# Kernel optimization log

Hardware: AMD Instinct MI355X
Metric: run time of the kernel (lower is better)

## Reference

```python
import jax, jax.numpy as jnp
import numpy as np
import math

R, C, B, E, H, F = 64, 256, 1, 768, 12, 3072
D = E // H  # head dim = 64
EPS = 1e-6  # flax LayerNorm default


def _ln(x, s, b):
    mu = jnp.mean(x, axis=-1, keepdims=True)
    var = jnp.mean((x - mu) ** 2, axis=-1, keepdims=True)
    return (x - mu) * jax.lax.rsqrt(var + EPS) * s + b


def setup_inputs() -> dict:
    key = jax.random.key(0)
    ks = jax.random.split(key, 16)
    w = lambda k, sh: jax.random.normal(k, sh, jnp.float32) * 0.02
    z = lambda sh: jnp.zeros(sh, jnp.float32)
    return {
        "x": jax.random.normal(ks[0], (R, C, B, E), jnp.float32),
        "ln1_s": jnp.ones((E,), jnp.float32), "ln1_b": z((E,)),
        "r_wq": w(ks[1], (E, E)), "r_bq": z((E,)),
        "r_wk": w(ks[2], (E, E)), "r_bk": z((E,)),
        "r_wv": w(ks[3], (E, E)), "r_bv": z((E,)),
        "r_wo": w(ks[4], (E, E)), "r_bo": z((E,)),
        "ln2_s": jnp.ones((E,), jnp.float32), "ln2_b": z((E,)),
        "c_wq": w(ks[5], (E, E)), "c_bq": z((E,)),
        "c_wk": w(ks[6], (E, E)), "c_bk": z((E,)),
        "c_wv": w(ks[7], (E, E)), "c_bv": z((E,)),
        "c_wo": w(ks[8], (E, E)), "c_bo": z((E,)),
        "ln3_s": jnp.ones((E,), jnp.float32), "ln3_b": z((E,)),
        "f_w1": w(ks[9], (E, F)), "f_b1": z((F,)),
        "f_w2": w(ks[10], (F, E)), "f_b2": z((E,)),
    }


def reference(x, ln1_s, ln1_b, r_wq, r_bq, r_wk, r_bk, r_wv, r_bv, r_wo, r_bo,
              ln2_s, ln2_b, c_wq, c_bq, c_wk, c_bk, c_wv, c_bv, c_wo, c_bo,
              ln3_s, ln3_b, f_w1, f_b1, f_w2, f_b2):
    qkv = (R, C, B, H, D)
    # --- tied row self-attention (NOTE: original code has no residual adds) ---
    h = _ln(x, ln1_s, ln1_b)
    q = (h @ r_wq + r_bq).reshape(qkv) * (D ** -0.5 / math.sqrt(R))  # tied-row scaling
    k = (h @ r_wk + r_bk).reshape(qkv)
    v = (h @ r_wv + r_bv).reshape(qkv)
    aw = jnp.einsum('rinhd,rjnhd->hnij', q, k)  # single softmax tied across rows
    ap = jax.nn.softmax(aw, axis=-1)
    ctx = jnp.einsum('hnij,rjnhd->rinhd', ap, v).reshape(R, C, B, E)
    x = ctx @ r_wo + r_bo
    # --- column self-attention (per-column attention over rows) ---
    h = _ln(x, ln2_s, ln2_b)
    q = (h @ c_wq + c_bq).reshape(qkv) * (D ** -0.5)
    k = (h @ c_wk + c_bk).reshape(qkv)
    v = (h @ c_wv + c_bv).reshape(qkv)
    aw = jnp.einsum('icnhd,jcnhd->hcnij', q, k)
    ap = jax.nn.softmax(aw, axis=-1)
    ctx = jnp.einsum('hcnij,jcnhd->icnhd', ap, v).reshape(R, C, B, E)
    x = ctx @ c_wo + c_bo
    # --- FFN (gelu approximate=True matches flax default) ---
    h = _ln(x, ln3_s, ln3_b)
    return jax.nn.gelu(h @ f_w1 + f_b1) @ f_w2 + f_b2
```

## Files before the change

kernel.cpp:

```cpp
#include <hip/hip_runtime.h>
#include <hip/hip_bf16.h>
#include <stdint.h>
#include <stddef.h>

#define R_ 64
#define C_ 256
#define E_ 768
#define H_ 12
#define F_ 3072
#define D_ 64
#define NT_ (R_*C_)
#define HCRD_ ((size_t)H_*C_*R_*D_)

typedef float f32x4 __attribute__((ext_vector_type(4)));
typedef __bf16 bf16x8 __attribute__((ext_vector_type(8)));
typedef unsigned short us4 __attribute__((ext_vector_type(4)));
typedef unsigned short us8 __attribute__((ext_vector_type(8)));

typedef __attribute__((address_space(3))) uint32_t lds_u32;
typedef __attribute__((address_space(1))) uint32_t glb_u32;

__device__ __forceinline__ void gld16(const uint16_t* g, uint16_t* l) {
  __builtin_amdgcn_global_load_lds((const glb_u32*)g, (lds_u32*)l, 16, 0, 0);
}

__device__ __forceinline__ uint16_t f2b(float f) {
  __bf16 h = (__bf16)f;
  return *(uint16_t*)&h;
}

#define VM_WAIT4 { asm volatile("s_waitcnt vmcnt(4)" ::: "memory"); __builtin_amdgcn_sched_barrier(0); }
#define VM_WAIT0 { asm volatile("s_waitcnt vmcnt(0)" ::: "memory"); __builtin_amdgcn_sched_barrier(0); }
#define BARRIER  { __builtin_amdgcn_s_barrier(); __builtin_amdgcn_sched_barrier(0); }

enum { EP_F32B = 0, EP_GELU = 1, EP_AW = 2, EP_CTX = 3, EP_QKVROW = 4, EP_QKVCOL = 5 };

template<int EP, bool SWZ, bool PERM>
__global__ __launch_bounds__(256)
void gemm_bt(const uint16_t* __restrict__ A, const uint16_t* __restrict__ B,
             const float* __restrict__ bias, const float* __restrict__ biasK,
             const float* __restrict__ biasV, void* __restrict__ out,
             int M, int N, int K, int lda, int ldb, long sAz, long sBz, float scale)
{
  __shared__ uint16_t As[3][4096];
  __shared__ uint16_t Bs[3][4096];
  const int tid  = threadIdx.x;
  const int wave = tid >> 6, lane = tid & 63;
  const int z = blockIdx.z;

  int bx = blockIdx.x, by = blockIdx.y;
  if constexpr (SWZ) {
    int lin = blockIdx.x + gridDim.x * blockIdx.y;
    const int q = (gridDim.x * gridDim.y) >> 3;
    const int wid = (lin & 7) * q + (lin >> 3);
    bx = wid % gridDim.x; by = wid / gridDim.x;
  }

  const long bm = (long)by * 128;
  int kc = 0; long bnb = bx;
  if constexpr (EP == EP_AW) { kc = bx & 3; bnb = bx >> 2; }
  const long bn = bnb * 128;
  const uint16_t* Bb = B + (long)z * sBz + bn * (long)ldb + (long)kc * 1024;
  const int wr = (wave >> 1) * 64;
  const int wc = (wave & 1) * 64;
  const int lr = lane & 15;
  const int lq = lane >> 4;

  const int t0 = tid, t1 = tid + 256;
  const int ar0 = t0 >> 2, ar1 = t1 >> 2;
  const int ac0 = (((t0 & 3) ^ ((ar0 >> 1) & 3)) * 8);
  const int ac1 = (((t1 & 3) ^ ((ar1 >> 1) & 3)) * 8);

  long am0 = bm + ar0, am1 = bm + ar1;
  if constexpr (PERM) {
    am0 = ((am0 & 63) << 8) | (am0 >> 6);
    am1 = ((am1 & 63) << 8) | (am1 >> 6);
  }
  const uint16_t* a0p = A + (long)z * sAz + am0 * (long)lda + (long)kc * 1024;
  const uint16_t* a1p = A + (long)z * sAz + am1 * (long)lda + (long)kc * 1024;
  const uint16_t* b0p = Bb + (long)ar0 * ldb;
  const uint16_t* b1p = Bb + (long)ar1 * ldb;

  auto STAGE = [&](int bi, int kt) {
    gld16(a0p + kt + ac0, &As[bi][t0 * 8]);
    gld16(a1p + kt + ac1, &As[bi][t1 * 8]);
    gld16(b0p + kt + ac0, &Bs[bi][t0 * 8]);
    gld16(b1p + kt + ac1, &Bs[bi][t1 * 8]);
  };

  int apos[4], bpos[4];
#pragma unroll
  for (int i = 0; i < 4; ++i) {
    const int ra = wr + i * 16 + lr;
    const int rb = wc + i * 16 + lr;
    apos[i] = ra * 32 + (lq ^ ((ra >> 1) & 3)) * 8;
    bpos[i] = rb * 32 + (lq ^ ((rb >> 1) & 3)) * 8;
  }

  f32x4 acc[4][4];
#pragma unroll
  for (int i = 0; i < 4; ++i)
#pragma unroll
    for (int j = 0; j < 4; ++j) acc[i][j] = (f32x4){0.f, 0.f, 0.f, 0.f};

  const int nt = K >> 5;
  STAGE(0, 0);
  if (nt > 1) { STAGE(1, 32); VM_WAIT4; } else { VM_WAIT0; }
  BARRIER;

  int cur = 0;
  for (int t = 0; t < nt; ++t) {
    if (t + 2 < nt) {
      int sl = cur + 2; if (sl >= 3) sl -= 3;
      STAGE(sl, (t + 2) << 5);
    }

    bf16x8 af[4], bfm[4];
#pragma unroll
    for (int i = 0; i < 4; ++i) {
      af[i]  = *(const bf16x8*)&As[cur][apos[i]];
      bfm[i] = *(const bf16x8*)&Bs[cur][bpos[i]];
    }
    __builtin_amdgcn_s_setprio(1);
#pragma unroll
    for (int mi = 0; mi < 4; ++mi)
#pragma unroll
      for (int ni = 0; ni < 4; ++ni)
        acc[mi][ni] = __builtin_amdgcn_mfma_f32_16x16x32_bf16(af[mi], bfm[ni], acc[mi][ni], 0, 0, 0);
    __builtin_amdgcn_s_setprio(0);

    if (t + 2 < nt)      { VM_WAIT4; BARRIER; }
    else if (t + 1 < nt) { VM_WAIT0; BARRIER; }
    cur = (cur == 2) ? 0 : cur + 1;
  }
  __syncthreads();

  if constexpr (EP == EP_F32B) {
#pragma unroll
    for (int mi = 0; mi < 4; ++mi)
#pragma unroll
      for (int ni = 0; ni < 4; ++ni)
#pragma unroll
        for (int r = 0; r < 4; ++r) {
          const long row = bm + wr + mi * 16 + lq * 4 + r;
          const long col = bn + wc + ni * 16 + lr;
          ((float*)out)[row * N + col] = acc[mi][ni][r] + bias[col];
        }
  } else if constexpr (EP == EP_AW) {
#pragma unroll
    for (int mi = 0; mi < 4; ++mi)
#pragma unroll
      for (int ni = 0; ni < 4; ++ni)
#pragma unroll
        for (int r = 0; r < 4; ++r) {
          const long row = bm + wr + mi * 16 + lq * 4 + r;
          const long col = bn + wc + ni * 16 + lr;
          ((float*)out)[((long)(z * 4 + kc) * M + row) * N + col] = acc[mi][ni][r];
        }
  } else if constexpr (EP == EP_CTX) {
#pragma unroll
    for (int mi = 0; mi < 4; ++mi)
#pragma unroll
      for (int ni = 0; ni < 4; ++ni)
#pragma unroll
        for (int r = 0; r < 4; ++r) {
          const long row = bm + wr + mi * 16 + lq * 4 + r;
          const long col = bn + wc + ni * 16 + lr;
          ((uint16_t*)out)[((col >> 6) * C_ + row) * E_ + (long)z * 64 + (col & 63)] =
              f2b(acc[mi][ni][r]);
        }
  } else {
    uint16_t* slab = (wave < 3) ? &As[wave][0] : &Bs[0][0];
    const long colb = bn + wc;
    int grp = 0; long cc0 = colb;
    const float* bb = bias;
    if constexpr (EP != EP_GELU) {
      grp = colb >= 1536 ? 2 : (colb >= 768 ? 1 : 0);
      cc0 = colb - (long)grp * 768;
      bb = grp == 0 ? bias : (grp == 1 ? biasK : biasV);
    }
    const bool tr = (EP != EP_GELU) && (grp == 2);

#pragma unroll
    for (int mi = 0; mi < 4; ++mi)
#pragma unroll
      for (int ni = 0; ni < 4; ++ni)
#pragma unroll
        for (int r = 0; r < 4; ++r) {
          const int lrow = mi * 16 + lq * 4 + r;
          const int lcol = ni * 16 + lr;
          float val;
          if constexpr (EP == EP_GELU) {
            const float t = acc[mi][ni][r] + bias[colb + lcol];
            const float u = 0.7978845608028654f * (t + 0.044715f * t * t * t);
            const float e = __expf(2.f * u);
            val = 0.5f * t * (2.f - 2.f / (e + 1.f));
          } else {
            val = acc[mi][ni][r] + bb[cc0 + lcol];
            if (grp == 0) val *= scale;
          }
          const int sr = tr ? lcol : lrow;
          const int sc = tr ? lrow : lcol;
          const int psc = (sc & 7) | ((((sc >> 3) ^ (sr & 7))) << 3);
          slab[sr * 64 + psc] = f2b(val);
        }

    uint16_t* o16 = (uint16_t*)out;
    long obase, rstride;
    if constexpr (EP == EP_GELU) {
      obase = (bm + wr) * (long)N + colb; rstride = N;
    } else {
      const long h = cc0 >> 6;
      const long m0 = bm + wr;
      if constexpr (EP == EP_QKVROW) {
        const long rr = m0 >> 8, c0 = m0 & 255;
        if (grp < 2) { obase = (size_t)grp * HCRD_ + ((h * C_ + c0) * R_ + rr) * D_; rstride = R_ * D_; }
        else         { obase = 2 * HCRD_ + ((h * R_ + rr) * D_) * C_ + c0;           rstride = C_; }
      } else {
        const long cq = m0 >> 6;
        if (grp < 2) { obase = (size_t)grp * HCRD_ + ((h * C_ + cq) * R_) * D_; rstride = D_; }
        else         { obase = 2 * HCRD_ + ((h * C_ + cq) * D_) * R_;           rstride = R_; }
      }
    }

    const int rl = lane >> 3, chn = lane & 7;
#pragma unroll
    for (int pp = 0; pp < 8; ++pp) {
      const int srow = pp * 8 + rl;
      const int pch = chn ^ (srow & 7);
      us8 wv = *(const us8*)&slab[srow * 64 + pch * 8];
      *(us8*)(o16 + obase + (long)srow * rstride + chn * 8) = wv;
    }
  }
}

__global__ __launch_bounds__(256)
void ln_k(const float* __restrict__ x, const float* __restrict__ s, const float* __restrict__ b,
          uint16_t* __restrict__ out)
{
  const int wave = threadIdx.x >> 6, lane = threadIdx.x & 63;
  const long row = (long)blockIdx.x * 4 + wave;
  const float* xr = x + row * E_;
  f32x4 v[3];
  float sum = 0.f, sq = 0.f;
#pragma unroll
  for (int i = 0; i < 3; ++i) {
    v[i] = *(const f32x4*)(xr + (i * 64 + lane) * 4);
#pragma unroll
    for (int j = 0; j < 4; ++j) { sum += v[i][j]; sq += v[i][j] * v[i][j]; }
  }
#pragma unroll
  for (int m = 1; m < 64; m <<= 1) { sum += __shfl_xor(sum, m); sq += __shfl_xor(sq, m); }
  const float mu = sum * (1.f / E_);
  const float var = sq * (1.f / E_) - mu * mu;
  const float rs = rsqrtf(var + 1e-6f);
  uint16_t* orow = out + row * E_;
#pragma unroll
  for (int i = 0; i < 3; ++i) {
    const int e0 = (i * 64 + lane) * 4;
    us4 o;
#pragma unroll
    for (int j = 0; j < 4; ++j) o[j] = f2b((v[i][j] - mu) * rs * s[e0 + j] + b[e0 + j]);
    *(us4*)(orow + e0) = o;
  }
}

__global__ __launch_bounds__(256)
void softmax_k4(const float* __restrict__ aw4, uint16_t* __restrict__ ap)
{
  const int wave = threadIdx.x >> 6, lane = threadIdx.x & 63;
  const long row = (long)blockIdx.x * 4 + wave;
  const long h = row >> 8, i = row & 255;
  f32x4 v = (f32x4){0.f, 0.f, 0.f, 0.f};
#pragma unroll
  for (int kc = 0; kc < 4; ++kc) {
    f32x4 t = *(const f32x4*)(aw4 + (((h * 4 + kc) * C_ + i) * C_) + lane * 4);
#pragma unroll
    for (int j = 0; j < 4; ++j) v[j] += t[j];
  }
  float m = fmaxf(fmaxf(v[0], v[1]), fmaxf(v[2], v[3]));
#pragma unroll
  for (int k = 1; k < 64; k <<= 1) m = fmaxf(m, __shfl_xor(m, k));
  f32x4 e; float s = 0.f;
#pragma unroll
  for (int j = 0; j < 4; ++j) { e[j] = __expf(v[j] - m); s += e[j]; }
#pragma unroll
  for (int k = 1; k < 64; k <<= 1) s += __shfl_xor(s, k);
  const float inv = 1.f / s;
  us4 o;
#pragma unroll
  for (int j = 0; j < 4; ++j) o[j] = f2b(e[j] * inv);
  *(us4*)(ap + row * C_ + lane * 4) = o;
}

__global__ __launch_bounds__(256)
void tcvt(const float* __restrict__ in, uint16_t* __restrict__ out, int K, int N)
{
  __shared__ float t[32][33];
  const int tx = threadIdx.x, ty = threadIdx.y;
  const long k0 = (long)blockIdx.y * 32, n0 = (long)blockIdx.x * 32;
  for (int i = ty; i < 32; i += 8) t[i][tx] = in[(k0 + i) * N + n0 + tx];
  __syncthreads();
  for (int i = ty; i < 32; i += 8) out[(n0 + i) * K + k0 + tx] = f2b(t[tx][i]);
}

__global__ __launch_bounds__(64)
void colattn(const uint16_t* __restrict__ q, const uint16_t* __restrict__ k,
             const uint16_t* __restrict__ v, uint16_t* __restrict__ ctx)
{
  __shared__ uint16_t Qs[64 * 64];
  __shared__ uint16_t Ks[64 * 64];
  __shared__ uint16_t Vs[64 * 64];
  const int hc = blockIdx.x;
  const int h = hc >> 8, c = hc & 255;
  const int lane = threadIdx.x;
  const uint16_t* qb = q + (long)hc * (R_ * D_);
  const uint16_t* kb = k + (long)hc * (R_ * D_);
  const uint16_t* vb = v + (long)hc * (D_ * R_);
#pragma unroll
  for (int it = 0; it < 8; ++it) {
    const int o = (it * 64 + lane) * 8;
    gld16(qb + o, &Qs[o]);
    gld16(kb + o, &Ks[o]);
    gld16(vb + o, &Vs[o]);
  }
  asm volatile("s_waitcnt vmcnt(0)" ::: "memory");
  __builtin_amdgcn_sched_barrier(0);

  const int lr = lane & 15, lq = lane >> 4;
  f32x4 acc[4][4];
#pragma unroll
  for (int i = 0; i < 4; ++i)
#pragma unroll
    for (int j = 0; j < 4; ++j) acc[i][j] = (f32x4){0.f, 0.f, 0.f, 0.f};

#pragma unroll
  for (int kt = 0; kt < 2; ++kt) {
    bf16x8 af[4], bfm[4];
#pragma unroll
    for (int i = 0; i < 4; ++i) {
      af[i]  = *(const bf16x8*)&Qs[(i * 16 + lr) * 64 + kt * 32 + lq * 8];
      bfm[i] = *(const bf16x8*)&Ks[(i * 16 + lr) * 64 + kt * 32 + lq * 8];
    }
#pragma unroll
    for (int mi = 0; mi < 4; ++mi)
#pragma unroll
      for (int ni = 0; ni < 4; ++ni)
        acc[mi][ni] = __builtin_amdgcn_mfma_f32_16x16x32_bf16(af[mi], bfm[ni], acc[mi][ni], 0, 0, 0);
  }

#pragma unroll
  for (int mi = 0; mi < 4; ++mi) {
#pragma unroll
    for (int r = 0; r < 4; ++r) {
      float mx = fmaxf(fmaxf(acc[mi][0][r], acc[mi][1][r]), fmaxf(acc[mi][2][r], acc[mi][3][r]));
#pragma unroll
      for (int s = 1; s < 16; s <<= 1) mx = fmaxf(mx, __shfl_xor(mx, s));
      float e0 = __expf(acc[mi][0][r] - mx), e1 = __expf(acc[mi][1][r] - mx);
      float e2 = __expf(acc[mi][2][r] - mx), e3 = __expf(acc[mi][3][r] - mx);
      float sum = e0 + e1 + e2 + e3;
#pragma unroll
      for (int s = 1; s < 16; s <<= 1) sum += __shfl_xor(sum, s);
      const float inv = 1.f / sum;
      const int i = mi * 16 + lq * 4 + r;
      Qs[i * 64 +  0 + lr] = f2b(e0 * inv);
      Qs[i * 64 + 16 + lr] = f2b(e1 * inv);
      Qs[i * 64 + 32 + lr] = f2b(e2 * inv);
      Qs[i * 64 + 48 + lr] = f2b(e3 * inv);
    }
  }
  __syncthreads();

  f32x4 o_[4][4];
#pragma unroll
  for (int i = 0; i < 4; ++i)
#pragma unroll
    for (int j = 0; j < 4; ++j) o_[i][j] = (f32x4){0.f, 0.f, 0.f, 0.f};

#pragma unroll
  for (int kt = 0; kt < 2; ++kt) {
    bf16x8 pa[4], vv[4];
#pragma unroll
    for (int i = 0; i < 4; ++i) {
      pa[i] = *(const bf16x8*)&Qs[(i * 16 + lr) * 64 + kt * 32 + lq * 8];
      vv[i] = *(const bf16x8*)&Vs[(i * 16 + lr) * 64 + kt * 32 + lq * 8];
    }
#pragma unroll
    for (int mi = 0; mi < 4; ++mi)
#pragma unroll
      for (int ni = 0; ni < 4; ++ni)
        o_[mi][ni] = __builtin_amdgcn_mfma_f32_16x16x32_bf16(pa[mi], vv[ni], o_[mi][ni], 0, 0, 0);
  }

#pragma unroll
  for (int mi = 0; mi < 4; ++mi)
#pragma unroll
    for (int ni = 0; ni < 4; ++ni)
#pragma unroll
      for (int r = 0; r < 4; ++r) {
        const int i = mi * 16 + lq * 4 + r;
        const int d = ni * 16 + lr;
        ctx[((long)i * C_ + c) * E_ + h * 64 + d] = f2b(o_[mi][ni][r]);
      }
}

extern "C" void kernel_launch(void* const* d_in, const int* in_sizes, int n_in,
                              void* d_out, int out_size, void* d_ws, size_t ws_size,
                              hipStream_t stream)
{
  (void)in_sizes; (void)n_in; (void)out_size; (void)ws_size;
  const float* x     = (const float*)d_in[0];
  const float* ln1_s = (const float*)d_in[1];
  const float* ln1_b = (const float*)d_in[2];
  const float* r_wq  = (const float*)d_in[3];
  const float* r_bq  = (const float*)d_in[4];
  const float* r_wk  = (const float*)d_in[5];
  const float* r_bk  = (const float*)d_in[6];
  const float* r_wv  = (const float*)d_in[7];
  const float* r_bv  = (const float*)d_in[8];
  const float* r_wo  = (const float*)d_in[9];
  const float* r_bo  = (const float*)d_in[10];
  const float* ln2_s = (const float*)d_in[11];
  const float* ln2_b = (const float*)d_in[12];
  const float* c_wq  = (const float*)d_in[13];
  const float* c_bq  = (const float*)d_in[14];
  const float* c_wk  = (const float*)d_in[15];
  const float* c_bk  = (const float*)d_in[16];
  const float* c_wv  = (const float*)d_in[17];
  const float* c_bv  = (const float*)d_in[18];
  const float* c_wo  = (const float*)d_in[19];
  const float* c_bo  = (const float*)d_in[20];
  const float* ln3_s = (const float*)d_in[21];
  const float* ln3_b = (const float*)d_in[22];
  const float* f_w1  = (const float*)d_in[23];
  const float* f_b1  = (const float*)d_in[24];
  const float* f_w2  = (const float*)d_in[25];
  const float* f_b2  = (const float*)d_in[26];

  uint8_t* p = (uint8_t*)d_ws;
  auto take = [&p](size_t n) { uint8_t* r = p; p += (n + 255) & ~(size_t)255; return r; };

  uint16_t* wqkv1 = (uint16_t*)take((size_t)3 * E_ * E_ * 2);
  uint16_t* wqkv2 = (uint16_t*)take((size_t)3 * E_ * E_ * 2);
  uint16_t* rwoT  = (uint16_t*)take((size_t)E_ * E_ * 2);
  uint16_t* cwoT  = (uint16_t*)take((size_t)E_ * E_ * 2);
  uint16_t* w1T   = (uint16_t*)take((size_t)E_ * F_ * 2);
  uint16_t* w2T   = (uint16_t*)take((size_t)F_ * E_ * 2);
  uint16_t* hb    = (uint16_t*)take((size_t)NT_ * E_ * 2);
  uint16_t* qkvT  = (uint16_t*)take(3 * HCRD_ * 2);
  uint16_t* qT = qkvT, *kT = qkvT + HCRD_, *vT = qkvT + 2 * HCRD_;
  uint16_t* ctxb  = (uint16_t*)take((size_t)NT_ * E_ * 2);
  uint16_t* apb   = (uint16_t*)take((size_t)H_ * C_ * C_ * 2);
  uint16_t* g     = qkvT;
  float*    awb4  = (float*)ctxb;
  float*    x1    = (float*)d_out;

  const dim3 tb32(32, 8);
  const dim3 gEE(E_ / 32, E_ / 32);
  tcvt<<<gEE, tb32, 0, stream>>>(r_wq, wqkv1 + 0 * E_ * E_, E_, E_);
  tcvt<<<gEE, tb32, 0, stream>>>(r_wk, wqkv1 + 1 * E_ * E_, E_, E_);
  tcvt<<<gEE, tb32, 0, stream>>>(r_wv, wqkv1 + 2 * E_ * E_, E_, E_);
  tcvt<<<gEE, tb32, 0, stream>>>(c_wq, wqkv2 + 0 * E_ * E_, E_, E_);
  tcvt<<<gEE, tb32, 0, stream>>>(c_wk, wqkv2 + 1 * E_ * E_, E_, E_);
  tcvt<<<gEE, tb32, 0, stream>>>(c_wv, wqkv2 + 2 * E_ * E_, E_, E_);
  tcvt<<<gEE, tb32, 0, stream>>>(r_wo, rwoT, E_, E_);
  tcvt<<<gEE, tb32, 0, stream>>>(c_wo, cwoT, E_, E_);
  tcvt<<<dim3(F_ / 32, E_ / 32), tb32, 0, stream>>>(f_w1, w1T, E_, F_);
  tcvt<<<dim3(E_ / 32, F_ / 32), tb32, 0, stream>>>(f_w2, w2T, F_, E_);

  const dim3 gProj(E_ / 128, NT_ / 128, 1);
  const dim3 gQKV((3 * E_) / 128, NT_ / 128, 1);

  ln_k<<<NT_ / 4, 256, 0, stream>>>(x, ln1_s, ln1_b, hb);
  gemm_bt<EP_QKVROW, true, false><<<gQKV, 256, 0, stream>>>(hb, wqkv1, r_bq, r_bk, r_bv, qkvT,
      NT_, 3 * E_, E_, E_, E_, 0, 0, 0.015625f);
  gemm_bt<EP_AW, false, false><<<dim3(8, C_ / 128, H_), 256, 0, stream>>>(
      qT, kT, nullptr, nullptr, nullptr, awb4,
      C_, C_, 1024, R_ * D_, R_ * D_, (long)C_ * R_ * D_, (long)C_ * R_ * D_, 1.f);
  softmax_k4<<<(H_ * C_) / 4, 256, 0, stream>>>(awb4, apb);
  gemm_bt<EP_CTX, false, false><<<dim3((R_ * D_) / 128, C_ / 128, H_), 256, 0, stream>>>(
      apb, vT, nullptr, nullptr, nullptr,
      ctxb, C_, R_ * D_, C_, C_, C_, (long)C_ * C_, (long)R_ * D_ * C_, 1.f);
  gemm_bt<EP_F32B, true, false><<<gProj, 256, 0, stream>>>(ctxb, rwoT, r_bo, nullptr, nullptr, x1,
      NT_, E_, E_, E_, E_, 0, 0, 1.f);

  ln_k<<<NT_ / 4, 256, 0, stream>>>(x1, ln2_s, ln2_b, hb);
  gemm_bt<EP_QKVCOL, true, true><<<gQKV, 256, 0, stream>>>(hb, wqkv2, c_bq, c_bk, c_bv, qkvT,
      NT_, 3 * E_, E_, E_, E_, 0, 0, 0.125f);
  colattn<<<H_ * C_, 64, 0, stream>>>(qT, kT, vT, ctxb);
  gemm_bt<EP_F32B, true, false><<<gProj, 256, 0, stream>>>(ctxb, cwoT, c_bo, nullptr, nullptr, x1,
      NT_, E_, E_, E_, E_, 0, 0, 1.f);

  ln_k<<<NT_ / 4, 256, 0, stream>>>(x1, ln3_s, ln3_b, hb);
  gemm_bt<EP_GELU, true, false><<<dim3(F_ / 128, NT_ / 128, 1), 256, 0, stream>>>(
      hb, w1T, f_b1, nullptr, nullptr, g,
      NT_, F_, E_, E_, E_, 0, 0, 1.f);
  gemm_bt<EP_F32B, true, false><<<gProj, 256, 0, stream>>>(g, w2T, f_b2, nullptr, nullptr, d_out,
      NT_, E_, F_, F_, F_, 0, 0, 1.f);
}
```

Measured before the change: 596.6 us.

## Add 256x256-tile 8-wave GEMM kernel for projection, QKV and FFN GEMMs

Adds a gemm256 kernel using 512 threads, 256x256 output tiles and a K=64 double-buffered LDS pipeline. Each K step is split into four half-stages, with loads interleaved between MFMA groups. All large token-dimension GEMMs (QKV, output projections, FFN) now use it, which raises arithmetic intensity per block and cuts global traffic. The old 128-tile kernel is trimmed to only the batched attention GEMMs. The large tiles produce few blocks for the N=768 GEMMs (192 blocks), which may underfill the GPU, and they increase register pressure.

```diff
diff --git a/kernel.cpp b/kernel.cpp
--- a/kernel.cpp
+++ b/kernel.cpp
@@ -29,18 +29,221 @@
   return *(uint16_t*)&h;
 }
 
+#define VM_WAIT6 { asm volatile("s_waitcnt vmcnt(6)" ::: "memory"); __builtin_amdgcn_sched_barrier(0); }
 #define VM_WAIT4 { asm volatile("s_waitcnt vmcnt(4)" ::: "memory"); __builtin_amdgcn_sched_barrier(0); }
 #define VM_WAIT0 { asm volatile("s_waitcnt vmcnt(0)" ::: "memory"); __builtin_amdgcn_sched_barrier(0); }
 #define BARRIER  { __builtin_amdgcn_s_barrier(); __builtin_amdgcn_sched_barrier(0); }
 
 enum { EP_F32B = 0, EP_GELU = 1, EP_AW = 2, EP_CTX = 3, EP_QKVROW = 4, EP_QKVCOL = 5 };
 
-template<int EP, bool SWZ, bool PERM>
+template<int EP, bool PERM>
+__global__ __launch_bounds__(512, 2)
+void gemm256(const uint16_t* __restrict__ A, const uint16_t* __restrict__ B,
+             const float* __restrict__ bias, const float* __restrict__ biasK,
+             const float* __restrict__ biasV, void* __restrict__ out,
+             int N, int K, int lda, int ldb, float scale)
+{
+  __shared__ uint16_t lds[2][4][8192];
+  const int tid  = threadIdx.x;
+  const int wave = tid >> 6, lane = tid & 63;
+  const int wm = wave >> 2, wn = wave & 3;
+  const int lr = lane & 15, lq = lane >> 4;
+
+  int lin = blockIdx.x + gridDim.x * blockIdx.y;
+  const int q8 = (gridDim.x * gridDim.y) >> 3;
+  const int wid = (lin & 7) * q8 + (lin >> 3);
+  const int bx = wid % gridDim.x, by = wid / gridDim.x;
+  const long bm = (long)by * 256, bn = (long)bx * 256;
+
+  const int r0 = tid >> 2;
+  const int csw = (((tid & 3) ^ ((r0 >> 1) & 3)) * 8);
+  long am0 = bm + r0, am1 = bm + r0 + 128;
+  if constexpr (PERM) {
+    am0 = ((am0 & 63) << 8) | (am0 >> 6);
+    am1 = ((am1 & 63) << 8) | (am1 >> 6);
+  }
+  const uint16_t* aR0 = A + am0 * (long)lda + csw;
+  const uint16_t* aR1 = A + am1 * (long)lda + csw;
+  const uint16_t* bR0 = B + (bn + r0) * (long)ldb + csw;
+  const uint16_t* bR1 = B + (bn + r0 + 128) * (long)ldb + csw;
+
+  auto stageH = [&](int s) {
+    const int u = s >> 2, j = s & 3;
+    const int kb = u * 64 + (j >> 1) * 32;
+    uint16_t* d = &lds[u & 1][j][0];
+    if (j & 1) { gld16(aR0 + kb, d + tid * 8); gld16(aR1 + kb, d + (tid + 512) * 8); }
+    else       { gld16(bR0 + kb, d + tid * 8); gld16(bR1 + kb, d + (tid + 512) * 8); }
+  };
+  auto aoff = [&](int row) { return row * 32 + ((lq ^ ((row >> 1) & 3)) * 8); };
+
+  f32x4 acc[8][4];
+#pragma unroll
+  for (int i = 0; i < 8; ++i)
+#pragma unroll
+    for (int j = 0; j < 4; ++j) acc[i][j] = (f32x4){0.f, 0.f, 0.f, 0.f};
+
+  const int nt = K >> 6;
+  stageH(0); stageH(1); stageH(2); stageH(3);
+  VM_WAIT4;
+  stageH(4); stageH(5); stageH(6);
+  VM_WAIT6;
+  BARRIER;
+
+  for (int t = 0; t < nt; ++t) {
+    const int buf = t & 1;
+    const uint16_t* B0h = &lds[buf][0][0];
+    const uint16_t* A0h = &lds[buf][1][0];
+    const uint16_t* B1h = &lds[buf][2][0];
+    const uint16_t* A1h = &lds[buf][3][0];
+    const int s0 = 4 * t + 7;
+    bf16x8 af[4], bf[4];
+
+#pragma unroll
+    for (int i = 0; i < 4; ++i) {
+      bf[i] = *(const bf16x8*)&B0h[aoff(wn * 64 + i * 16 + lr)];
+      af[i] = *(const bf16x8*)&A0h[aoff(wm * 128 + i * 16 + lr)];
+    }
+    if (s0 < 4 * nt) stageH(s0);
+    BARRIER;
+    __builtin_amdgcn_s_setprio(1);
+#pragma unroll
+    for (int mi = 0; mi < 4; ++mi)
+#pragma unroll
+      for (int ni = 0; ni < 4; ++ni)
+        acc[mi][ni] = __builtin_amdgcn_mfma_f32_16x16x32_bf16(af[mi], bf[ni], acc[mi][ni], 0, 0, 0);
+    __builtin_amdgcn_s_setprio(0);
+    BARRIER;
+
+#pragma unroll
+    for (int i = 0; i < 4; ++i)
+      af[i] = *(const bf16x8*)&A0h[aoff(wm * 128 + 64 + i * 16 + lr)];
+    if (s0 + 1 < 4 * nt) stageH(s0 + 1);
+    BARRIER;
+    __builtin_amdgcn_s_setprio(1);
+#pragma unroll
+    for (int mi = 0; mi < 4; ++mi)
+#pragma unroll
+      for (int ni = 0; ni < 4; ++ni)
+        acc[4 + mi][ni] = __builtin_amdgcn_mfma_f32_16x16x32_bf16(af[mi], bf[ni], acc[4 + mi][ni], 0, 0, 0);
+    __builtin_amdgcn_s_setprio(0);
+    BARRIER;
+
+#pragma unroll
+    for (int i = 0; i < 4; ++i) {
+      bf[i] = *(const bf16x8*)&B1h[aoff(wn * 64 + i * 16 + lr)];
+      af[i] = *(const bf16x8*)&A1h[aoff(wm * 128 + i * 16 + lr)];
+    }
+    if (s0 + 2 < 4 * nt) stageH(s0 + 2);
+    BARRIER;
+    __builtin_amdgcn_s_setprio(1);
+#pragma unroll
+    for (int mi = 0; mi < 4; ++mi)
+#pragma unroll
+      for (int ni = 0; ni < 4; ++ni)
+        acc[mi][ni] = __builtin_amdgcn_mfma_f32_16x16x32_bf16(af[mi], bf[ni], acc[mi][ni], 0, 0, 0);
+    __builtin_amdgcn_s_setprio(0);
+    BARRIER;
+
+#pragma unroll
+    for (int i = 0; i < 4; ++i)
+      af[i] = *(const bf16x8*)&A1h[aoff(wm * 128 + 64 + i * 16 + lr)];
+    if (s0 + 3 < 4 * nt) stageH(s0 + 3);
+    BARRIER;
+    __builtin_amdgcn_s_setprio(1);
+#pragma unroll
+    for (int mi = 0; mi < 4; ++mi)
+#pragma unroll
+      for (int ni = 0; ni < 4; ++ni)
+        acc[4 + mi][ni] = __builtin_amdgcn_mfma_f32_16x16x32_bf16(af[mi], bf[ni], acc[4 + mi][ni], 0, 0, 0);
+    __builtin_amdgcn_s_setprio(0);
+    if (t < nt - 2)       VM_WAIT6
+    else if (t == nt - 2) VM_WAIT0
+    BARRIER;
+  }
+  __syncthreads();
+
+  if constexpr (EP == EP_F32B) {
+#pragma unroll
+    for (int mi = 0; mi < 8; ++mi)
+#pragma unroll
+      for (int ni = 0; ni < 4; ++ni)
+#pragma unroll
+        for (int r = 0; r < 4; ++r) {
+          const long row = bm + wm * 128 + mi * 16 + lq * 4 + r;
+          const long col = bn + wn * 64 + ni * 16 + lr;
+          ((float*)out)[row * N + col] = acc[mi][ni][r] + bias[col];
+        }
+  } else {
+    uint16_t* slabW = ((uint16_t*)lds) + (size_t)wave * 8192;
+    const long colb = bn + wn * 64;
+    int grp = 0; long cc0 = colb;
+    const float* bb = bias;
+    if constexpr (EP != EP_GELU) {
+      grp = colb >= 1536 ? 2 : (colb >= 768 ? 1 : 0);
+      cc0 = colb - (long)grp * 768;
+      bb = grp == 0 ? bias : (grp == 1 ? biasK : biasV);
+    }
+    const bool tr = (EP != EP_GELU) && (grp == 2);
+#pragma unroll
+    for (int sub = 0; sub < 2; ++sub) {
+      uint16_t* slab = slabW + sub * 4096;
+      const long m0 = bm + wm * 128 + sub * 64;
+#pragma unroll
+      for (int mi = 0; mi < 4; ++mi)
+#pragma unroll
+        for (int ni = 0; ni < 4; ++ni)
+#pragma unroll
+          for (int r = 0; r < 4; ++r) {
+            const int lrow = mi * 16 + lq * 4 + r;
+            const int lcol = ni * 16 + lr;
+            float val;
+            if constexpr (EP == EP_GELU) {
+              const float t = acc[sub * 4 + mi][ni][r] + bias[colb + lcol];
+              const float u = 0.7978845608028654f * (t + 0.044715f * t * t * t);
+              const float e = __expf(2.f * u);
+              val = 0.5f * t * (2.f - 2.f / (e + 1.f));
+            } else {
+              val = acc[sub * 4 + mi][ni][r] + bb[cc0 + lcol];
+              if (grp == 0) val *= scale;
+            }
+            const int sr = tr ? lcol : lrow;
+            const int sc = tr ? lrow : lcol;
+            const int psc = (sc & 7) | ((((sc >> 3) ^ (sr & 7))) << 3);
+            slab[sr * 64 + psc] = f2b(val);
+          }
+      uint16_t* o16 = (uint16_t*)out;
+      long obase, rstride;
+      if constexpr (EP == EP_GELU) {
+        obase = m0 * (long)N + colb; rstride = N;
+      } else {
+        const long h = cc0 >> 6;
+        if constexpr (EP == EP_QKVROW) {
+          const long rr = m0 >> 8, c0 = m0 & 255;
+          if (grp < 2) { obase = (size_t)grp * HCRD_ + ((h * C_ + c0) * R_ + rr) * D_; rstride = R_ * D_; }
+          else         { obase = 2 * HCRD_ + ((h * R_ + rr) * D_) * C_ + c0;           rstride = C_; }
+        } else {
+          const long cq = m0 >> 6;
+          if (grp < 2) { obase = (size_t)grp * HCRD_ + ((h * C_ + cq) * R_) * D_; rstride = D_; }
+          else         { obase = 2 * HCRD_ + ((h * C_ + cq) * D_) * R_;           rstride = R_; }
+        }
+      }
+      const int rl = lane >> 3, chn = lane & 7;
+#pragma unroll
+      for (int pp = 0; pp < 8; ++pp) {
+        const int srow = pp * 8 + rl;
+        const int pch = chn ^ (srow & 7);
+        us8 wv = *(const us8*)&slab[srow * 64 + pch * 8];
+        *(us8*)(o16 + obase + (long)srow * rstride + chn * 8) = wv;
+      }
+    }
+  }
+}
+
+template<int EP>
 __global__ __launch_bounds__(256)
 void gemm_bt(const uint16_t* __restrict__ A, const uint16_t* __restrict__ B,
-             const float* __restrict__ bias, const float* __restrict__ biasK,
-             const float* __restrict__ biasV, void* __restrict__ out,
-             int M, int N, int K, int lda, int ldb, long sAz, long sBz, float scale)
+             void* __restrict__ out,
+             int M, int N, int K, int lda, int ldb, long sAz, long sBz)
 {
   __shared__ uint16_t As[3][4096];
   __shared__ uint16_t Bs[3][4096];
@@ -48,19 +251,10 @@
   const int wave = tid >> 6, lane = tid & 63;
   const int z = blockIdx.z;
 
-  int bx = blockIdx.x, by = blockIdx.y;
-  if constexpr (SWZ) {
-    int lin = blockIdx.x + gridDim.x * blockIdx.y;
-    const int q = (gridDim.x * gridDim.y) >> 3;
-    const int wid = (lin & 7) * q + (lin >> 3);
-    bx = wid % gridDim.x; by = wid / gridDim.x;
-  }
-
-  const long bm = (long)by * 128;
-  int kc = 0; long bnb = bx;
-  if constexpr (EP == EP_AW) { kc = bx & 3; bnb = bx >> 2; }
+  const long bm = (long)blockIdx.y * 128;
+  int kc = 0; long bnb = blockIdx.x;
+  if constexpr (EP == EP_AW) { kc = blockIdx.x & 3; bnb = blockIdx.x >> 2; }
   const long bn = bnb * 128;
-  const uint16_t* Bb = B + (long)z * sBz + bn * (long)ldb + (long)kc * 1024;
   const int wr = (wave >> 1) * 64;
   const int wc = (wave & 1) * 64;
   const int lr = lane & 15;
@@ -71,15 +265,10 @@
   const int ac0 = (((t0 & 3) ^ ((ar0 >> 1) & 3)) * 8);
   const int ac1 = (((t1 & 3) ^ ((ar1 >> 1) & 3)) * 8);
 
-  long am0 = bm + ar0, am1 = bm + ar1;
-  if constexpr (PERM) {
-    am0 = ((am0 & 63) << 8) | (am0 >> 6);
-    am1 = ((am1 & 63) << 8) | (am1 >> 6);
-  }
-  const uint16_t* a0p = A + (long)z * sAz + am0 * (long)lda + (long)kc * 1024;
-  const uint16_t* a1p = A + (long)z * sAz + am1 * (long)lda + (long)kc * 1024;
-  const uint16_t* b0p = Bb + (long)ar0 * ldb;
-  const uint16_t* b1p = Bb + (long)ar1 * ldb;
+  const uint16_t* a0p = A + (long)z * sAz + (bm + ar0) * (long)lda + (long)kc * 1024;
+  const uint16_t* a1p = A + (long)z * sAz + (bm + ar1) * (long)lda + (long)kc * 1024;
+  const uint16_t* b0p = B + (long)z * sBz + (bn + ar0) * (long)ldb + (long)kc * 1024;
+  const uint16_t* b1p = B + (long)z * sBz + (bn + ar1) * (long)ldb + (long)kc * 1024;
 
   auto STAGE = [&](int bi, int kt) {
     gld16(a0p + kt + ac0, &As[bi][t0 * 8]);
@@ -114,7 +303,6 @@
       int sl = cur + 2; if (sl >= 3) sl -= 3;
       STAGE(sl, (t + 2) << 5);
     }
-
     bf16x8 af[4], bfm[4];
 #pragma unroll
     for (int i = 0; i < 4; ++i) {
@@ -133,105 +321,22 @@
     else if (t + 1 < nt) { VM_WAIT0; BARRIER; }
     cur = (cur == 2) ? 0 : cur + 1;
   }
-  __syncthreads();
-
-  if constexpr (EP == EP_F32B) {
-#pragma unroll
-    for (int mi = 0; mi < 4; ++mi)
-#pragma unroll
-      for (int ni = 0; ni < 4; ++ni)
-#pragma unroll
-        for (int r = 0; r < 4; ++r) {
-          const long row = bm + wr + mi * 16 + lq * 4 + r;
-          const long col = bn + wc + ni * 16 + lr;
-          ((float*)out)[row * N + col] = acc[mi][ni][r] + bias[col];
-        }
-  } else if constexpr (EP == EP_AW) {
-#pragma unroll
-    for (int mi = 0; mi < 4; ++mi)
-#pragma unroll
-      for (int ni = 0; ni < 4; ++ni)
-#pragma unroll
-        for (int r = 0; r < 4; ++r) {
-          const long row = bm + wr + mi * 16 + lq * 4 + r;
-          const long col = bn + wc + ni * 16 + lr;
+
+#pragma unroll
+  for (int mi = 0; mi < 4; ++mi)
+#pragma unroll
+    for (int ni = 0; ni < 4; ++ni)
+#pragma unroll
+      for (int r = 0; r < 4; ++r) {
+        const long row = bm + wr + mi * 16 + lq * 4 + r;
+        const long col = bn + wc + ni * 16 + lr;
+        if constexpr (EP == EP_AW) {
           ((float*)out)[((long)(z * 4 + kc) * M + row) * N + col] = acc[mi][ni][r];
-        }
-  } else if constexpr (EP == EP_CTX) {
-#pragma unroll
-    for (int mi = 0; mi < 4; ++mi)
-#pragma unroll
-      for (int ni = 0; ni < 4; ++ni)
-#pragma unroll
-        for (int r = 0; r < 4; ++r) {
-          const long row = bm + wr + mi * 16 + lq * 4 + r;
-          const long col = bn + wc + ni * 16 + lr;
+        } else {
           ((uint16_t*)out)[((col >> 6) * C_ + row) * E_ + (long)z * 64 + (col & 63)] =
               f2b(acc[mi][ni][r]);
         }
-  } else {
-    uint16_t* slab = (wave < 3) ? &As[wave][0] : &Bs[0][0];
-    const long colb = bn + wc;
-    int grp = 0; long cc0 = colb;
-    const float* bb = bias;
-    if constexpr (EP != EP_GELU) {
-      grp = colb >= 1536 ? 2 : (colb >= 768 ? 1 : 0);
-      cc0 = colb - (long)grp * 768;
-      bb = grp == 0 ? bias : (grp == 1 ? biasK : biasV);
-    }
-    const bool tr = (EP != EP_GELU) && (grp == 2);
-
-#pragma unroll
-    for (int mi = 0; mi < 4; ++mi)
-#pragma unroll
-      for (int ni = 0; ni < 4; ++ni)
-#pragma unroll
-        for (int r = 0; r < 4; ++r) {
-          const int lrow = mi * 16 + lq * 4 + r;
-          const int lcol = ni * 16 + lr;
-          float val;
-          if constexpr (EP == EP_GELU) {
-            const float t = acc[mi][ni][r] + bias[colb + lcol];
-            const float u = 0.7978845608028654f * (t + 0.044715f * t * t * t);
-            const float e = __expf(2.f * u);
-            val = 0.5f * t * (2.f - 2.f / (e + 1.f));
-          } else {
-            val = acc[mi][ni][r] + bb[cc0 + lcol];
-            if (grp == 0) val *= scale;
-          }
-          const int sr = tr ? lcol : lrow;
-          const int sc = tr ? lrow : lcol;
-          const int psc = (sc & 7) | ((((sc >> 3) ^ (sr & 7))) << 3);
-          slab[sr * 64 + psc] = f2b(val);
-        }
-
-    uint16_t* o16 = (uint16_t*)out;
-    long obase, rstride;
-    if constexpr (EP == EP_GELU) {
-      obase = (bm + wr) * (long)N + colb; rstride = N;
-    } else {
-      const long h = cc0 >> 6;
-      const long m0 = bm + wr;
-      if constexpr (EP == EP_QKVROW) {
-        const long rr = m0 >> 8, c0 = m0 & 255;
-        if (grp < 2) { obase = (size_t)grp * HCRD_ + ((h * C_ + c0) * R_ + rr) * D_; rstride = R_ * D_; }
-        else         { obase = 2 * HCRD_ + ((h * R_ + rr) * D_) * C_ + c0;           rstride = C_; }
-      } else {
-        const long cq = m0 >> 6;
-        if (grp < 2) { obase = (size_t)grp * HCRD_ + ((h * C_ + cq) * R_) * D_; rstride = D_; }
-        else         { obase = 2 * HCRD_ + ((h * C_ + cq) * D_) * R_;           rstride = R_; }
       }
-    }
-
-    const int rl = lane >> 3, chn = lane & 7;
-#pragma unroll
-    for (int pp = 0; pp < 8; ++pp) {
-      const int srow = pp * 8 + rl;
-      const int pch = chn ^ (srow & 7);
-      us8 wv = *(const us8*)&slab[srow * 64 + pch * 8];
-      *(us8*)(o16 + obase + (long)srow * rstride + chn * 8) = wv;
-    }
-  }
 }
 
 __global__ __launch_bounds__(256)
@@ -468,33 +573,27 @@
   tcvt<<<dim3(F_ / 32, E_ / 32), tb32, 0, stream>>>(f_w1, w1T, E_, F_);
   tcvt<<<dim3(E_ / 32, F_ / 32), tb32, 0, stream>>>(f_w2, w2T, F_, E_);
 
-  const dim3 gProj(E_ / 128, NT_ / 128, 1);
-  const dim3 gQKV((3 * E_) / 128, NT_ / 128, 1);
-
   ln_k<<<NT_ / 4, 256, 0, stream>>>(x, ln1_s, ln1_b, hb);
-  gemm_bt<EP_QKVROW, true, false><<<gQKV, 256, 0, stream>>>(hb, wqkv1, r_bq, r_bk, r_bv, qkvT,
-      NT_, 3 * E_, E_, E_, E_, 0, 0, 0.015625f);
-  gemm_bt<EP_AW, false, false><<<dim3(8, C_ / 128, H_), 256, 0, stream>>>(
-      qT, kT, nullptr, nullptr, nullptr, awb4,
-      C_, C_, 1024, R_ * D_, R_ * D_, (long)C_ * R_ * D_, (long)C_ * R_ * D_, 1.f);
+  gemm256<EP_QKVROW, false><<<dim3(9, 64), 512, 0, stream>>>(
+      hb, wqkv1, r_bq, r_bk, r_bv, qkvT, 3 * E_, E_, E_, E_, 0.015625f);
+  gemm_bt<EP_AW><<<dim3(8, 2, H_), 256, 0, stream>>>(
+      qT, kT, awb4, C_, C_, 1024, R_ * D_, R_ * D_, (long)C_ * R_ * D_, (long)C_ * R_ * D_);
   softmax_k4<<<(H_ * C_) / 4, 256, 0, stream>>>(awb4, apb);
-  gemm_bt<EP_CTX, false, false><<<dim3((R_ * D_) / 128, C_ / 128, H_), 256, 0, stream>>>(
-      apb, vT, nullptr, nullptr, nullptr,
-      ctxb, C_, R_ * D_, C_, C_, C_, (long)C_ * C_, (long)R_ * D_ * C_, 1.f);
-  gemm_bt<EP_F32B, true, false><<<gProj, 256, 0, stream>>>(ctxb, rwoT, r_bo, nullptr, nullptr, x1,
-      NT_, E_, E_, E_, E_, 0, 0, 1.f);
+  gemm_bt<EP_CTX><<<dim3((R_ * D_) / 128, 2, H_), 256, 0, stream>>>(
+      apb, vT, ctxb, C_, R_ * D_, C_, C_, C_, (long)C_ * C_, (long)R_ * D_ * C_);
+  gemm256<EP_F32B, false><<<dim3(3, 64), 512, 0, stream>>>(
+      ctxb, rwoT, r_bo, nullptr, nullptr, x1, E_, E_, E_, E_, 1.f);
 
   ln_k<<<NT_ / 4, 256, 0, stream>>>(x1, ln2_s, ln2_b, hb);
-  gemm_bt<EP_QKVCOL, true, true><<<gQKV, 256, 0, stream>>>(hb, wqkv2, c_bq, c_bk, c_bv, qkvT,
-      NT_, 3 * E_, E_, E_, E_, 0, 0, 0.125f);
+  gemm256<EP_QKVCOL, true><<<dim3(9, 64), 512, 0, stream>>>(
+      hb, wqkv2, c_bq, c_bk, c_bv, qkvT, 3 * E_, E_, E_, E_, 0.125f);
   colattn<<<H_ * C_, 64, 0, stream>>>(qT, kT, vT, ctxb);
-  gemm_bt<EP_F32B, true, false><<<gProj, 256, 0, stream>>>(ctxb, cwoT, c_bo, nullptr, nullptr, x1,
-      NT_, E_, E_, E_, E_, 0, 0, 1.f);
+  gemm256<EP_F32B, false><<<dim3(3, 64), 512, 0, stream>>>(
+      ctxb, cwoT, c_bo, nullptr, nullptr, x1, E_, E_, E_, E_, 1.f);
 
   ln_k<<<NT_ / 4, 256, 0, stream>>>(x1, ln3_s, ln3_b, hb);
-  gemm_bt<EP_GELU, true, false><<<dim3(F_ / 128, NT_ / 128, 1), 256, 0, stream>>>(
-      hb, w1T, f_b1, nullptr, nullptr, g,
-      NT_, F_, E_, E_, E_, 0, 0, 1.f);
-  gemm_bt<EP_F32B, true, false><<<gProj, 256, 0, stream>>>(g, w2T, f_b2, nullptr, nullptr, d_out,
-      NT_, E_, F_, F_, F_, 0, 0, 1.f);
-}
+  gemm256<EP_GELU, false><<<dim3(12, 64), 512, 0, stream>>>(
+      hb, w1T, f_b1, nullptr, nullptr, g, F_, E_, E_, E_, 1.f);
+  gemm256<EP_F32B, false><<<dim3(3, 64), 512, 0, stream>>>(
+      g, w2T, f_b2, nullptr, nullptr, d_out, E_, F_, F_, F_, 1.f);
+}
```

Result: faster. 574.2 us (-3.8%).
